# Kernel optimization log

Hardware: AMD Instinct MI355X
Metric: run time of the kernel (lower is better)

Reference implementation:

```python
import jax, jax.numpy as jnp
import numpy as np

B, T, D, H = 8, 2048, 1024, 64

def setup_inputs() -> dict:
    key = jax.random.key(0)
    kx, kq, kk, kv = jax.random.split(key, 4)
    x = jax.random.normal(kx, (B, T, D), dtype=jnp.float32)
    # Linear(embd_size, head_size, bias=False) weights, stored as [D, H] for x @ W
    Wq = jax.random.normal(kq, (D, H), dtype=jnp.float32) * (D ** -0.5)
    Wk = jax.random.normal(kk, (D, H), dtype=jnp.float32) * (D ** -0.5)
    Wv = jax.random.normal(kv, (D, H), dtype=jnp.float32) * (D ** -0.5)
    return {"x": x, "Wq": Wq, "Wk": Wk, "Wv": Wv}

def reference(x, Wq, Wk, Wv):
    Tcur = x.shape[1]
    q = x @ Wq  # [B, T, H]
    k = x @ Wk
    v = x @ Wv
    scores = jnp.einsum('bth,bsh->bts', q, k)
    # NOTE: faithful to source quirk: scores are MULTIPLIED by sqrt(T)
    scores = scores * (Tcur ** 0.5)
    causal = jnp.tril(jnp.ones((Tcur, Tcur), dtype=bool))
    scores = jnp.where(causal, scores, -jnp.inf)
    attn = jax.nn.softmax(scores, axis=2)  # dropout p=0.0 -> identity
    return jnp.einsum('bts,bsh->bth', attn, v)
```

## Files before the change

### kernel.cpp

```cpp
#include <hip/hip_runtime.h>
#include <hip/hip_bf16.h>

#define BB 8
#define TT 2048
#define DD 1024
#define HH 64
#define NROWS (BB*TT)
#define SCALE 45.25483399593904f
#define SPLIT 4

typedef __attribute__((ext_vector_type(8))) short short8;
typedef __attribute__((ext_vector_type(4))) float f32x4;

__device__ inline ushort bf16rne(float f) {
    unsigned u = __float_as_uint(f);
    return (ushort)((u + 0x7fffu + ((u >> 16) & 1u)) >> 16);
}
__device__ inline void bfsplit(float f, ushort& hi, ushort& lo) {
    hi = bf16rne(f);
    float fh = __uint_as_float(((unsigned)hi) << 16);
    lo = bf16rne(f - fh);
}
__device__ inline void split_pack8(const float* v, int4& h4, int4& l4) {
    ushort h[8], l[8];
    #pragma unroll
    for (int j = 0; j < 8; ++j) bfsplit(v[j], h[j], l[j]);
    h4 = make_int4((int)(h[0] | ((unsigned)h[1] << 16)), (int)(h[2] | ((unsigned)h[3] << 16)),
                   (int)(h[4] | ((unsigned)h[5] << 16)), (int)(h[6] | ((unsigned)h[7] << 16)));
    l4 = make_int4((int)(l[0] | ((unsigned)l[1] << 16)), (int)(l[2] | ((unsigned)l[3] << 16)),
                   (int)(l[4] | ((unsigned)l[5] << 16)), (int)(l[6] | ((unsigned)l[7] << 16)));
}

__device__ inline void gload_lds16(const void* g, void* l) {
    __builtin_amdgcn_global_load_lds(
        (const __attribute__((address_space(1))) unsigned int*)(uintptr_t)(g),
        (__attribute__((address_space(3))) unsigned int*)(uintptr_t)(l),
        16, 0, 0);
}

__global__ __launch_bounds__(256) void wprep_kernel(
        const float* __restrict__ Wq, const float* __restrict__ Wk,
        const float* __restrict__ Wv,
        ushort* __restrict__ WpHi, ushort* __restrict__ WpLo) {
    __shared__ float ws[64 * 65];
    const int m = blockIdx.x >> 4;
    const int c = blockIdx.x & 15;
    const float* W = (m == 0) ? Wq : (m == 1) ? Wk : Wv;
    const int tid = threadIdx.x;

    #pragma unroll
    for (int p = 0; p < 4; ++p) {
        int i = tid + p * 256;
        int r = i >> 4, q4 = i & 15;
        float4 v = *(const float4*)(W + (size_t)(c * 64 + r) * 64 + q4 * 4);
        ws[r * 65 + q4 * 4 + 0] = v.x;
        ws[r * 65 + q4 * 4 + 1] = v.y;
        ws[r * 65 + q4 * 4 + 2] = v.z;
        ws[r * 65 + q4 * 4 + 3] = v.w;
    }
    __syncthreads();

    #pragma unroll
    for (int p = 0; p < 2; ++p) {
        int gi = tid + p * 256;
        int nn = gi >> 3, g8 = gi & 7;
        int o  = g8 ^ (nn & 7);
        float v[8];
        #pragma unroll
        for (int j = 0; j < 8; ++j) v[j] = ws[(o * 8 + j) * 65 + nn];
        int4 h4, l4; split_pack8(v, h4, l4);
        size_t base = (size_t)c * 12288 + (size_t)(m * 64 + nn) * 64 + g8 * 8;
        *(int4*)(WpHi + base) = h4;
        *(int4*)(WpLo + base) = l4;
    }
}

__global__ __launch_bounds__(512) void qkv_kernel(
        const float* __restrict__ x,
        const ushort* __restrict__ WpHi, const ushort* __restrict__ WpLo,
        float* __restrict__ Qo, ushort* __restrict__ KhiP,
        ushort* __restrict__ KloP, ushort* __restrict__ VtP) {
    __shared__ ushort Ahi[2][64 * 64], Alo[2][64 * 64];
    __shared__ ushort Bhi[2][192 * 64], Blo[2][192 * 64];
    const int tid  = threadIdx.x;
    const int lane = tid & 63;
    const int w    = tid >> 6;
    const int wm   = w >> 2;
    const int wn   = w & 3;
    const int n15  = lane & 15;
    const int g    = lane >> 4;
    const int csw  = n15 & 7;
    const int row0 = blockIdx.x * 64;

    f32x4 acc[2][3];
    #pragma unroll
    for (int ms = 0; ms < 2; ++ms)
        #pragma unroll
        for (int nt = 0; nt < 3; ++nt) acc[ms][nt] = (f32x4)0.f;

    const int ar = tid >> 3, aoc = tid & 7;
    const float* xrow = x + (size_t)(row0 + ar) * 1024 + aoc * 8;
    const int adi = ar * 64 + ((aoc ^ (ar & 7)) << 3);

    const ushort* wsh = WpHi + (size_t)lane * 8;
    const ushort* wsl = WpLo + (size_t)lane * 8;

    {
        float v[8];
        *(float4*)v       = *(const float4*)(xrow);
        *(float4*)(v + 4) = *(const float4*)(xrow + 4);
        int4 h4, l4; split_pack8(v, h4, l4);
        *(int4*)&Ahi[0][adi] = h4;
        *(int4*)&Alo[0][adi] = l4;
    }
    #pragma unroll
    for (int p = 0; p < 3; ++p) {
        int j = w * 3 + p;
        gload_lds16(wsh + j * 512, &Bhi[0][j * 512]);
        gload_lds16(wsl + j * 512, &Blo[0][j * 512]);
    }
    float xA[8], xB[8];
    *(float4*)(xA)     = *(const float4*)(xrow + 64);
    *(float4*)(xA + 4) = *(const float4*)(xrow + 68);
    *(float4*)(xB)     = *(const float4*)(xrow + 128);
    *(float4*)(xB + 4) = *(const float4*)(xrow + 132);
    __syncthreads();

    int cur = 0;
    for (int c = 0; c < 16; ++c) {
        const int c3 = (c + 3 < 16) ? c + 3 : 15;
        float xN[8];
        *(float4*)(xN)     = *(const float4*)(xrow + c3 * 64);
        *(float4*)(xN + 4) = *(const float4*)(xrow + c3 * 64 + 4);
        const int c1 = (c + 1 < 16) ? c + 1 : 15;
        {
            const ushort* sh = wsh + (size_t)c1 * 12288;
            const ushort* sl = wsl + (size_t)c1 * 12288;
            #pragma unroll
            for (int p = 0; p < 3; ++p) {
                int j = w * 3 + p;
                gload_lds16(sh + j * 512, &Bhi[cur ^ 1][j * 512]);
                gload_lds16(sl + j * 512, &Blo[cur ^ 1][j * 512]);
            }
        }
        {
            int4 h4, l4; split_pack8(xA, h4, l4);
            *(int4*)&Ahi[cur ^ 1][adi] = h4;
            *(int4*)&Alo[cur ^ 1][adi] = l4;
        }
        #pragma unroll
        for (int kh = 0; kh < 2; ++kh) {
            short8 afh[2], afl[2], bfh[3], bfl[3];
            #pragma unroll
            for (int ms = 0; ms < 2; ++ms) {
                int ao = (wm * 32 + ms * 16 + n15) * 64 + (((4 * kh + g) ^ csw) << 3);
                afh[ms] = *(const short8*)&Ahi[cur][ao];
                afl[ms] = *(const short8*)&Alo[cur][ao];
            }
            #pragma unroll
            for (int nt = 0; nt < 3; ++nt) {
                int bo = (wn * 48 + nt * 16 + n15) * 64 + (((4 * kh + g) ^ csw) << 3);
                bfh[nt] = *(const short8*)&Bhi[cur][bo];
                bfl[nt] = *(const short8*)&Blo[cur][bo];
            }
            #pragma unroll
            for (int nt = 0; nt < 3; ++nt)
                #pragma unroll
                for (int ms = 0; ms < 2; ++ms) {
                    acc[ms][nt] = __builtin_amdgcn_mfma_f32_16x16x32_bf16(
                        afh[ms], bfh[nt], acc[ms][nt], 0, 0, 0);
                    acc[ms][nt] = __builtin_amdgcn_mfma_f32_16x16x32_bf16(
                        afl[ms], bfh[nt], acc[ms][nt], 0, 0, 0);
                    acc[ms][nt] = __builtin_amdgcn_mfma_f32_16x16x32_bf16(
                        afh[ms], bfl[nt], acc[ms][nt], 0, 0, 0);
                }
        }
        __syncthreads();
        #pragma unroll
        for (int j = 0; j < 8; ++j) { xA[j] = xB[j]; xB[j] = xN[j]; }
        cur ^= 1;
    }

    const int b  = row0 >> 11;
    const int t0 = row0 & 2047;
    #pragma unroll
    for (int nt = 0; nt < 3; ++nt) {
        const int col = wn * 48 + nt * 16 + n15;
        const int mat = col >> 6;
        const int h   = col & 63;
        #pragma unroll
        for (int ms = 0; ms < 2; ++ms) {
            const int mb = row0 + wm * 32 + ms * 16 + 4 * g;
            if (mat == 0) {
                #pragma unroll
                for (int r = 0; r < 4; ++r)
                    Qo[(size_t)(mb + r) * 64 + h] = acc[ms][nt][r];
            } else if (mat == 1) {
                #pragma unroll
                for (int r = 0; r < 4; ++r) {
                    ushort hi, lo; bfsplit(acc[ms][nt][r], hi, lo);
                    KhiP[(size_t)(mb + r) * 64 + h] = hi;
                    KloP[(size_t)(mb + r) * 64 + h] = lo;
                }
            } else {
                ushort pk[4];
                #pragma unroll
                for (int r = 0; r < 4; ++r) pk[r] = bf16rne(acc[ms][nt][r]);
                const int tloc = t0 + wm * 32 + ms * 16 + 4 * g;
                *(uint2*)&VtP[((size_t)(b * 64 + h)) * 2048 + tloc] =
                    make_uint2(pk[0] | ((unsigned)pk[1] << 16),
                               pk[2] | ((unsigned)pk[3] << 16));
            }
        }
    }
}

__global__ __launch_bounds__(128) void attn_kernel(
        const float* __restrict__ Q, const ushort* __restrict__ Khi,
        const ushort* __restrict__ Klo, const ushort* __restrict__ Vt,
        float* __restrict__ Pacc, float* __restrict__ Pm,
        float* __restrict__ Pl) {
    __shared__ ushort KhiL[64 * 64];
    __shared__ ushort KloL[64 * 64];
    __shared__ ushort VtL[64 * 64];
    const int tid  = threadIdx.x;
    const int lane = tid & 63;
    const int w    = tid >> 6;
    const int n    = lane & 15;
    const int g    = lane >> 4;
    const int b    = blockIdx.y;
    const int xx   = blockIdx.x;
    const int qt   = 63 - (xx >> 2);
    const int sp   = xx & 3;
    const int q0   = qt * 32;
    const int qmin = q0 + w * 16;
    const int qrow = qmin + n;
    const int csw  = n & 7;
    const int ntiles = (q0 >> 6) + 1;
    const int it0  = (ntiles * sp) >> 2;
    const int it1  = (ntiles * (sp + 1)) >> 2;

    short8 qhi0, qhi1, qlo0, qlo1;
    {
        const float* qp = Q + ((size_t)b * TT + qrow) * HH + 8 * g;
        float v0[8], v1[8];
        *(float4*)(v0)     = *(const float4*)(qp);
        *(float4*)(v0 + 4) = *(const float4*)(qp + 4);
        *(float4*)(v1)     = *(const float4*)(qp + 32);
        *(float4*)(v1 + 4) = *(const float4*)(qp + 36);
        #pragma unroll
        for (int j = 0; j < 8; ++j) {
            ushort hi, lo;
            bfsplit(v0[j], hi, lo); qhi0[j] = (short)hi; qlo0[j] = (short)lo;
            bfsplit(v1[j], hi, lo); qhi1[j] = (short)hi; qlo1[j] = (short)lo;
        }
    }

    f32x4 accO[4];
    #pragma unroll
    for (int t = 0; t < 4; ++t) accO[t] = (f32x4)0.f;
    float m = -1e30f, l = 0.f;

    const ushort* gkh = Khi + (size_t)b * TT * HH;
    const ushort* gkl = Klo + (size_t)b * TT * HH;
    const ushort* gvt = Vt + (size_t)b * 64 * TT;

    const int crow = lane >> 3;
    const int coct = lane & 7;

    for (int it = it0; it < it1; ++it) {
        const int kb = it * 64;
        __syncthreads();
        #pragma unroll
        for (int p = 0; p < 4; ++p) {
            const int cc  = w * 4 + p;
            const int row = (cc << 3) + crow;
            const int soc = coct ^ (row & 7);
            gload_lds16(gkh + (size_t)(kb + row) * HH + (soc << 3), &KhiL[cc << 9]);
            gload_lds16(gkl + (size_t)(kb + row) * HH + (soc << 3), &KloL[cc << 9]);
            gload_lds16(gvt + (size_t)row * TT + kb + (soc << 3),   &VtL[cc << 9]);
        }
        __syncthreads();

        f32x4 s4[4];
        #pragma unroll
        for (int s = 0; s < 4; ++s) {
            const int keyl = 16 * s + n;
            const ushort* kbase = &KhiL[keyl << 6];
            const ushort* lbase = &KloL[keyl << 6];
            short8 kh0 = *(const short8*)(kbase + ((g ^ csw) << 3));
            short8 kh1 = *(const short8*)(kbase + (((4 + g) ^ csw) << 3));
            short8 kl0 = *(const short8*)(lbase + ((g ^ csw) << 3));
            short8 kl1 = *(const short8*)(lbase + (((4 + g) ^ csw) << 3));
            f32x4 a = (f32x4)0.f;
            a = __builtin_amdgcn_mfma_f32_16x16x32_bf16(kh0, qhi0, a, 0, 0, 0);
            a = __builtin_amdgcn_mfma_f32_16x16x32_bf16(kh1, qhi1, a, 0, 0, 0);
            a = __builtin_amdgcn_mfma_f32_16x16x32_bf16(kl0, qhi0, a, 0, 0, 0);
            a = __builtin_amdgcn_mfma_f32_16x16x32_bf16(kl1, qhi1, a, 0, 0, 0);
            a = __builtin_amdgcn_mfma_f32_16x16x32_bf16(kh0, qlo0, a, 0, 0, 0);
            a = __builtin_amdgcn_mfma_f32_16x16x32_bf16(kh1, qlo1, a, 0, 0, 0);
            s4[s] = a;
        }

        float sm[16];
        if (kb + 63 > qmin) {
            #pragma unroll
            for (int s = 0; s < 4; ++s)
                #pragma unroll
                for (int r = 0; r < 4; ++r) {
                    int keyg = kb + 16 * s + 4 * g + r;
                    sm[s * 4 + r] = (keyg <= qrow) ? s4[s][r] * SCALE : -1e30f;
                }
        } else {
            #pragma unroll
            for (int s = 0; s < 4; ++s)
                #pragma unroll
                for (int r = 0; r < 4; ++r) sm[s * 4 + r] = s4[s][r] * SCALE;
        }
        float pm = sm[0];
        #pragma unroll
        for (int i = 1; i < 16; ++i) pm = fmaxf(pm, sm[i]);
        pm = fmaxf(pm, __shfl_xor(pm, 16));
        pm = fmaxf(pm, __shfl_xor(pm, 32));
        float mn = fmaxf(m, pm);
        float es = __expf(m - mn);
        float p[16], ps = 0.f;
        #pragma unroll
        for (int i = 0; i < 16; ++i) { p[i] = __expf(sm[i] - mn); ps += p[i]; }
        ps += __shfl_xor(ps, 16);
        ps += __shfl_xor(ps, 32);
        l = l * es + ps;
        m = mn;
        #pragma unroll
        for (int t = 0; t < 4; ++t)
            #pragma unroll
            for (int r = 0; r < 4; ++r) accO[t][r] *= es;

        short8 pf0, pf1;
        #pragma unroll
        for (int j = 0; j < 4; ++j) {
            pf0[j]     = (short)bf16rne(p[0 * 4 + j]);
            pf0[j + 4] = (short)bf16rne(p[1 * 4 + j]);
            pf1[j]     = (short)bf16rne(p[2 * 4 + j]);
            pf1[j + 4] = (short)bf16rne(p[3 * 4 + j]);
        }

        #pragma unroll
        for (int t = 0; t < 4; ++t) {
            const int h = 16 * t + n;
            const ushort* vb = &VtL[h << 6];
            union { int2 d[2]; short8 v; } u0, u1;
            u0.d[0] = *(const int2*)(vb + ((4 * g) ^ (csw << 3)));
            u0.d[1] = *(const int2*)(vb + ((16 + 4 * g) ^ (csw << 3)));
            u1.d[0] = *(const int2*)(vb + ((32 + 4 * g) ^ (csw << 3)));
            u1.d[1] = *(const int2*)(vb + ((48 + 4 * g) ^ (csw << 3)));
            accO[t] = __builtin_amdgcn_mfma_f32_16x16x32_bf16(u0.v, pf0, accO[t], 0, 0, 0);
            accO[t] = __builtin_amdgcn_mfma_f32_16x16x32_bf16(u1.v, pf1, accO[t], 0, 0, 0);
        }
    }

    const size_t brow = (size_t)b * TT + qrow;
    float* pa = Pacc + ((size_t)sp * NROWS + brow) * 64 + 4 * g;
    #pragma unroll
    for (int t = 0; t < 4; ++t)
        *(f32x4*)(pa + 16 * t) = accO[t];
    if (g == 0) {
        Pm[(size_t)sp * NROWS + brow] = m;
        Pl[(size_t)sp * NROWS + brow] = l;
    }
}

__global__ __launch_bounds__(256) void combine_kernel(
        const float* __restrict__ Pacc, const float* __restrict__ Pm,
        const float* __restrict__ Pl, float* __restrict__ out) {
    const int u    = blockIdx.x * 256 + threadIdx.x;
    const int row  = u >> 2;
    const int quad = u & 3;

    float ms[SPLIT], ls[SPLIT], M = -1e30f;
    #pragma unroll
    for (int s = 0; s < SPLIT; ++s) {
        ms[s] = Pm[(size_t)s * NROWS + row];
        ls[s] = Pl[(size_t)s * NROWS + row];
        M = fmaxf(M, ms[s]);
    }
    float wgt[SPLIT], den = 0.f;
    #pragma unroll
    for (int s = 0; s < SPLIT; ++s) {
        wgt[s] = __expf(ms[s] - M);
        den += wgt[s] * ls[s];
    }
    const float inv = 1.0f / den;

    float4 o[4];
    #pragma unroll
    for (int i = 0; i < 4; ++i) o[i] = make_float4(0.f, 0.f, 0.f, 0.f);
    #pragma unroll
    for (int s = 0; s < SPLIT; ++s) {
        const float4* a = (const float4*)(Pacc + ((size_t)s * NROWS + row) * 64 + quad * 16);
        #pragma unroll
        for (int i = 0; i < 4; ++i) {
            float4 v = a[i];
            o[i].x += wgt[s] * v.x; o[i].y += wgt[s] * v.y;
            o[i].z += wgt[s] * v.z; o[i].w += wgt[s] * v.w;
        }
    }
    float4* op = (float4*)(out + (size_t)row * 64 + quad * 16);
    #pragma unroll
    for (int i = 0; i < 4; ++i)
        op[i] = make_float4(o[i].x * inv, o[i].y * inv, o[i].z * inv, o[i].w * inv);
}

extern "C" void kernel_launch(void* const* d_in, const int* in_sizes, int n_in,
                              void* d_out, int out_size, void* d_ws, size_t ws_size,
                              hipStream_t stream) {
    const float* x  = (const float*)d_in[0];
    const float* Wq = (const float*)d_in[1];
    const float* Wk = (const float*)d_in[2];
    const float* Wv = (const float*)d_in[3];
    float* outp = (float*)d_out;

    float*  Qw   = (float*)d_ws;
    ushort* KhiP = (ushort*)(Qw + (size_t)NROWS * HH);
    ushort* KloP = KhiP + (size_t)NROWS * HH;
    ushort* VtP  = KloP + (size_t)NROWS * HH;
    ushort* WpHi = VtP + (size_t)NROWS * HH;
    ushort* WpLo = WpHi + (size_t)3 * 64 * 1024;
    float*  Pacc = (float*)(WpLo + (size_t)3 * 64 * 1024);
    float*  Pm   = Pacc + (size_t)SPLIT * NROWS * HH;
    float*  Pl   = Pm + (size_t)SPLIT * NROWS;

    wprep_kernel<<<48, 256, 0, stream>>>(Wq, Wk, Wv, WpHi, WpLo);
    qkv_kernel<<<NROWS / 64, 512, 0, stream>>>(x, WpHi, WpLo, Qw, KhiP, KloP, VtP);
    attn_kernel<<<dim3(64 * SPLIT, BB), 128, 0, stream>>>(Qw, KhiP, KloP, VtP,
                                                          Pacc, Pm, Pl);
    combine_kernel<<<NROWS * 4 / 256, 256, 0, stream>>>(Pacc, Pm, Pl, outp);
}
```

Before: 72.03 us.

## Single-buffer x tile in QKV kernel with explicit waitcnt-based pipelining

The QKV projection kernel drops the double-buffered A (x) tiles in LDS and the three-deep register prefetch of x. Each iteration now splits and stores the current x chunk into a single LDS buffer, then issues the next chunk's global load. Synchronisation uses manual s_waitcnt vmcnt/lgkmcnt plus raw s_barrier and sched_barrier. This lowers LDS and register use and tightens the schedule, but x load latency is less hidden because the prefetch distance drops from three chunks to one. The hand-counted vmcnt(6) is fragile if the compiler emits a different number of outstanding loads.

Measured after the change: 71.20 us. No clear change (-1.2%).

```diff
diff --git a/kernel.cpp b/kernel.cpp
--- a/kernel.cpp
+++ b/kernel.cpp
@@ -80,7 +80,7 @@
         const ushort* __restrict__ WpHi, const ushort* __restrict__ WpLo,
         float* __restrict__ Qo, ushort* __restrict__ KhiP,
         ushort* __restrict__ KloP, ushort* __restrict__ VtP) {
-    __shared__ ushort Ahi[2][64 * 64], Alo[2][64 * 64];
+    __shared__ ushort Ahi[64 * 64], Alo[64 * 64];
     __shared__ ushort Bhi[2][192 * 64], Blo[2][192 * 64];
     const int tid  = threadIdx.x;
     const int lane = tid & 63;
@@ -105,33 +105,18 @@
     const ushort* wsh = WpHi + (size_t)lane * 8;
     const ushort* wsl = WpLo + (size_t)lane * 8;
 
-    {
-        float v[8];
-        *(float4*)v       = *(const float4*)(xrow);
-        *(float4*)(v + 4) = *(const float4*)(xrow + 4);
-        int4 h4, l4; split_pack8(v, h4, l4);
-        *(int4*)&Ahi[0][adi] = h4;
-        *(int4*)&Alo[0][adi] = l4;
-    }
     #pragma unroll
     for (int p = 0; p < 3; ++p) {
         int j = w * 3 + p;
         gload_lds16(wsh + j * 512, &Bhi[0][j * 512]);
         gload_lds16(wsl + j * 512, &Blo[0][j * 512]);
     }
-    float xA[8], xB[8];
-    *(float4*)(xA)     = *(const float4*)(xrow + 64);
-    *(float4*)(xA + 4) = *(const float4*)(xrow + 68);
-    *(float4*)(xB)     = *(const float4*)(xrow + 128);
-    *(float4*)(xB + 4) = *(const float4*)(xrow + 132);
-    __syncthreads();
+    float xv[8];
+    *(float4*)(xv)     = *(const float4*)(xrow);
+    *(float4*)(xv + 4) = *(const float4*)(xrow + 4);
 
     int cur = 0;
     for (int c = 0; c < 16; ++c) {
-        const int c3 = (c + 3 < 16) ? c + 3 : 15;
-        float xN[8];
-        *(float4*)(xN)     = *(const float4*)(xrow + c3 * 64);
-        *(float4*)(xN + 4) = *(const float4*)(xrow + c3 * 64 + 4);
         const int c1 = (c + 1 < 16) ? c + 1 : 15;
         {
             const ushort* sh = wsh + (size_t)c1 * 12288;
@@ -143,19 +128,30 @@
                 gload_lds16(sl + j * 512, &Blo[cur ^ 1][j * 512]);
             }
         }
+        asm volatile("s_waitcnt vmcnt(6)" ::: "memory");
+        __builtin_amdgcn_sched_barrier(0);
         {
-            int4 h4, l4; split_pack8(xA, h4, l4);
-            *(int4*)&Ahi[cur ^ 1][adi] = h4;
-            *(int4*)&Alo[cur ^ 1][adi] = l4;
-        }
+            int4 h4, l4; split_pack8(xv, h4, l4);
+            *(int4*)&Ahi[adi] = h4;
+            *(int4*)&Alo[adi] = l4;
+        }
+        {
+            const float* src = xrow + (size_t)c1 * 64;
+            *(float4*)(xv)     = *(const float4*)(src);
+            *(float4*)(xv + 4) = *(const float4*)(src + 4);
+        }
+        asm volatile("s_waitcnt lgkmcnt(0)" ::: "memory");
+        __builtin_amdgcn_s_barrier();
+        __builtin_amdgcn_sched_barrier(0);
+
         #pragma unroll
         for (int kh = 0; kh < 2; ++kh) {
             short8 afh[2], afl[2], bfh[3], bfl[3];
             #pragma unroll
             for (int ms = 0; ms < 2; ++ms) {
                 int ao = (wm * 32 + ms * 16 + n15) * 64 + (((4 * kh + g) ^ csw) << 3);
-                afh[ms] = *(const short8*)&Ahi[cur][ao];
-                afl[ms] = *(const short8*)&Alo[cur][ao];
+                afh[ms] = *(const short8*)&Ahi[ao];
+                afl[ms] = *(const short8*)&Alo[ao];
             }
             #pragma unroll
             for (int nt = 0; nt < 3; ++nt) {
@@ -175,9 +171,7 @@
                         afh[ms], bfl[nt], acc[ms][nt], 0, 0, 0);
                 }
         }
-        __syncthreads();
-        #pragma unroll
-        for (int j = 0; j < 8; ++j) { xA[j] = xB[j]; xB[j] = xN[j]; }
+        __builtin_amdgcn_s_barrier();
         cur ^= 1;
     }
 
```
